# Kernel tuning notes

Measured on AMD Instinct MI355X. Metric: run time of the kernel, lower is better.

## Reference

```python
import jax, jax.numpy as jnp
import numpy as np

N_IMG = 1024
N_VIEWS = 90


def _bilinear(img, yi, xi):
    """Bilinear sample img at float coords (yi=row, xi=col); 0 outside (skimage warp cval=0)."""
    n = img.shape[0]
    y0 = jnp.floor(yi)
    x0 = jnp.floor(xi)
    wy = yi - y0
    wx = xi - x0
    y0i = y0.astype(jnp.int32)
    x0i = x0.astype(jnp.int32)

    def get(yy, xx):
        valid = (yy >= 0) & (yy < n) & (xx >= 0) & (xx < n)
        v = img[jnp.clip(yy, 0, n - 1), jnp.clip(xx, 0, n - 1)]
        return jnp.where(valid, v, jnp.zeros((), img.dtype))

    v00 = get(y0i, x0i)
    v01 = get(y0i, x0i + 1)
    v10 = get(y0i + 1, x0i)
    v11 = get(y0i + 1, x0i + 1)
    return (v00 * (1 - wy) * (1 - wx) + v01 * (1 - wy) * wx
            + v10 * wy * (1 - wx) + v11 * wy * wx)


def radon_jax(image, theta_deg):
    """skimage.transform.radon(image, theta, circle=True) equivalent.
    Rotate image by each angle (bilinear, about center = N//2, inverse map as in
    skimage warp) and sum over rows. Returns sinogram [N, n_angles]."""
    n = image.shape[0]
    center = n // 2
    ang = jnp.deg2rad(theta_deg.astype(image.dtype))
    cos_a = jnp.cos(ang)  # [A]
    sin_a = jnp.sin(ang)
    coords = jnp.arange(n, dtype=image.dtype)
    X, Y = jnp.meshgrid(coords, coords)  # X = col (x), Y = row (y), [N, N]

    def rotate_and_sum(ca, sa):
        # inverse map: src = R @ dst (homogeneous, (x, y) order) as in skimage radon
        x_in = ca * X + sa * Y - center * (ca + sa - 1)
        y_in = -sa * X + ca * Y - center * (ca - sa - 1)
        rotated = _bilinear(image, y_in, x_in)  # [N, N]
        return rotated.sum(axis=0)  # sum over rows -> projection [N]

    sino = jax.vmap(rotate_and_sum)(cos_a, sin_a)  # [A, N]
    return sino.T  # [N, A] to match skimage radon layout


def setup_inputs() -> dict:
    key = jax.random.key(0)
    k1, _ = jax.random.split(key)
    x = jax.random.normal(k1, (N_IMG, N_IMG), dtype=jnp.float32)
    theta = jnp.arange(N_VIEWS, dtype=jnp.float32) * 2.0  # 0..178 deg, 2-deg spacing
    return {"x": x, "theta": theta}


def reference(x, theta):
    return radon_jax(x, theta)
```

## Files before the change

kernel.cpp:

```cpp
#include <hip/hip_runtime.h>

#define N_IMG    1024
#define N_VIEWS  90
#define CENTER   512
#define NTHREADS 256
#define NWAVES   4
#define NJOBS    8
#define BUFW     5120

typedef float v2f __attribute__((ext_vector_type(2)));

__device__ __forceinline__ void map_coords(float ca, float sa, float cx, float cy,
                                           float Xf, float Yf,
                                           float& x_in, float& y_in) {
    const float fx0 = fmaf(ca, Xf, cx);
    const float fy0 = fmaf(-sa, Xf, cy);
    x_in = fmaf(sa, Yf, fx0);
    y_in = fmaf(ca, Yf, fy0);
}

__device__ __forceinline__ void gload_lds4(const float* g, float* l) {
    __builtin_amdgcn_global_load_lds((const __attribute__((address_space(1))) void*)g,
                                     (__attribute__((address_space(3))) void*)l, 4, 0, 0);
}

__global__ __launch_bounds__(NTHREADS, 8) void radon_q(const float* __restrict__ img,
                                                       const float* __restrict__ theta,
                                                       float* __restrict__ out) {
    __shared__ float buf[BUFW];

    const int tx = blockIdx.x;
    const int q  = blockIdx.y;
    const int a  = blockIdx.z;
    const int X0 = tx * 64;
    const int Yq = q * (NJOBS * 32);
    const int tid  = threadIdx.x;
    const int lane = tid & 63;
    const int wv   = tid >> 6;

    const float ang = theta[a] * 0.017453292519943295f;
    float sa, ca;
    __sincosf(ang, &sa, &ca);
    const float cx = (float)CENTER * (1.0f - ca - sa);
    const float cy = (float)CENTER * (1.0f - ca + sa);

    const float Xf  = (float)(X0 + lane);
    const float fx0 = fmaf(ca, Xf, cx);
    const float fy0 = fmaf(-sa, Xf, cy);
    const v2f sa2 = {sa, sa};
    const v2f ca2 = {ca, ca};
    const v2f fx2 = {fx0, fx0};
    const v2f fy2 = {fy0, fy0};
    float acc = 0.0f;

    for (int j = 0; j < NJOBS; ++j) {
        const float Y0f = (float)(Yq + j * 32);
        const float Y1f = Y0f + 31.0f;
        float x00, y00, x01, y01, x10, y10, x11, y11;
        map_coords(ca, sa, cx, cy, (float)X0,        Y0f, x00, y00);
        map_coords(ca, sa, cx, cy, (float)(X0 + 63), Y0f, x01, y01);
        map_coords(ca, sa, cx, cy, (float)X0,        Y1f, x10, y10);
        map_coords(ca, sa, cx, cy, (float)(X0 + 63), Y1f, x11, y11);
        const float xmin = fminf(fminf(x00, x01), fminf(x10, x11));
        const float xmax = fmaxf(fmaxf(x00, x01), fmaxf(x10, x11));
        const float ymin = fminf(fminf(y00, y01), fminf(y10, y11));
        const float ymax = fmaxf(fmaxf(y00, y01), fmaxf(y10, y11));
        const int ix0 = (int)floorf(xmin);
        const int ix1 = (int)floorf(xmax) + 1;
        const int iy0 = (int)floorf(ymin);
        const int iy1 = (int)floorf(ymax) + 1;

        if (ix1 < 0 || ix0 > N_IMG - 1 || iy1 < 0 || iy0 > N_IMG - 1)
            continue;

        const bool interior = (ix0 >= 0) && (ix1 <= N_IMG - 1) &&
                              (iy0 >= 0) && (iy1 <= N_IMG - 1);
        const int win = ix0;
        const int WS  = ix1 - ix0 + 1;
        const int P   = WS | 1;
        const int R   = iy1 - iy0 + 1;

        if (interior) {
            const float* g = img + (size_t)(iy0 + wv) * N_IMG + win;
            float* l = buf + wv * P;
            if (WS <= 64) {
                for (int r = wv; r < R; r += NWAVES) {
                    if (lane < WS) gload_lds4(g + lane, l);
                    g += NWAVES * N_IMG;
                    l += NWAVES * P;
                }
            } else {
                for (int r = wv; r < R; r += NWAVES) {
                    gload_lds4(g + lane, l);
                    if (lane < WS - 64) gload_lds4(g + 64 + lane, l + 64);
                    g += NWAVES * N_IMG;
                    l += NWAVES * P;
                }
            }
        } else {
            for (int r = wv; r < R; r += NWAVES) {
                const int gy = iy0 + r;
                const bool rok = ((unsigned)gy < (unsigned)N_IMG);
                const float* gp = img + (size_t)gy * N_IMG;
                float* l = buf + r * P;
                const int gx = win + lane;
                if (lane < WS) {
                    if (rok && (unsigned)gx < (unsigned)N_IMG) gload_lds4(gp + gx, l);
                    else l[lane] = 0.0f;
                }
                if (WS > 64) {
                    const int gx2 = gx + 64;
                    if (lane < WS - 64) {
                        if (rok && (unsigned)gx2 < (unsigned)N_IMG) gload_lds4(gp + gx2, l + 64);
                        else l[64 + lane] = 0.0f;
                    }
                }
            }
        }
        __syncthreads();

        const float Yb = Y0f + (float)(wv * 8);
        const float Pf = (float)P;
        const v2f P2 = {Pf, Pf};
        const float basef = -(float)(iy0 * P + win);
        const v2f b2 = {basef, basef};
        v2f Y2 = {Yb, Yb + 1.0f};
        const v2f two2 = {2.0f, 2.0f};
        v2f acc2 = {0.0f, 0.0f};
        #pragma unroll
        for (int p = 0; p < 4; ++p) {
            const v2f x2 = sa2 * Y2 + fx2;
            const v2f y2 = ca2 * Y2 + fy2;
            v2f x0f = {floorf(x2.x), floorf(x2.y)};
            v2f y0f = {floorf(y2.x), floorf(y2.y)};
            const v2f wx = x2 - x0f;
            const v2f wy = y2 - y0f;
            const v2f lif = y0f * P2 + x0f + b2;
            const int li0 = (int)lif.x;
            const int li1 = (int)lif.y;
            const int li0p = li0 + P;
            const int li1p = li1 + P;
            const v2f t00 = {buf[li0],      buf[li1]};
            const v2f t01 = {buf[li0 + 1],  buf[li1 + 1]};
            const v2f t10 = {buf[li0p],     buf[li1p]};
            const v2f t11 = {buf[li0p + 1], buf[li1p + 1]};
            const v2f top = (t01 - t00) * wx + t00;
            const v2f bot = (t11 - t10) * wx + t10;
            acc2 += (bot - top) * wy + top;
            Y2 += two2;
        }
        acc += acc2.x + acc2.y;

        __syncthreads();
    }

    buf[tid] = acc;
    __syncthreads();
    if (tid < 64) {
        const float s = buf[tid] + buf[tid + 64] + buf[tid + 128] + buf[tid + 192];
        atomicAdd(&out[(size_t)(X0 + tid) * N_VIEWS + a], s);
    }
}

extern "C" void kernel_launch(void* const* d_in, const int* in_sizes, int n_in,
                              void* d_out, int out_size, void* d_ws, size_t ws_size,
                              hipStream_t stream) {
    const float* img   = (const float*)d_in[0];
    const float* theta = (const float*)d_in[1];
    float* out = (float*)d_out;
    (void)d_ws; (void)ws_size;

    (void)hipMemsetAsync(d_out, 0, (size_t)out_size * sizeof(float), stream);
    radon_q<<<dim3(16, 4, N_VIEWS), NTHREADS, 0, stream>>>(img, theta, out);
}
```

Before: 144.6 us.

## Halve per-job row tile to 16 and pad LDS stride to 32/64/96

Each job now covers 16 output rows instead of 32, with twice as many jobs per block, so the staged rotated footprint per job is smaller. The LDS row pitch becomes a power-of-two-like bucket (32/64/96) instead of WS|1. Narrow windows load two rows per wave so all 64 lanes issue loads. Bounding-box corners are precomputed outside the loop. The cost is twice as many barriers per block and possible LDS bank conflicts from even strides.

```diff
diff --git a/kernel.cpp b/kernel.cpp
--- a/kernel.cpp
+++ b/kernel.cpp
@@ -5,7 +5,7 @@
 #define CENTER   512
 #define NTHREADS 256
 #define NWAVES   4
-#define NJOBS    8
+#define NJOBS    16
 #define BUFW     5120
 
 typedef float v2f __attribute__((ext_vector_type(2)));
@@ -33,7 +33,7 @@
     const int q  = blockIdx.y;
     const int a  = blockIdx.z;
     const int X0 = tx * 64;
-    const int Yq = q * (NJOBS * 32);
+    const int Yq = q * (NJOBS * 16);
     const int tid  = threadIdx.x;
     const int lane = tid & 63;
     const int wv   = tid >> 6;
@@ -43,6 +43,11 @@
     __sincosf(ang, &sa, &ca);
     const float cx = (float)CENTER * (1.0f - ca - sa);
     const float cy = (float)CENTER * (1.0f - ca + sa);
+
+    const float fxA = fmaf(ca, (float)X0,        cx);
+    const float fxB = fmaf(ca, (float)(X0 + 63), cx);
+    const float fyA = fmaf(-sa, (float)X0,        cy);
+    const float fyB = fmaf(-sa, (float)(X0 + 63), cy);
 
     const float Xf  = (float)(X0 + lane);
     const float fx0 = fmaf(ca, Xf, cx);
@@ -54,13 +59,12 @@
     float acc = 0.0f;
 
     for (int j = 0; j < NJOBS; ++j) {
-        const float Y0f = (float)(Yq + j * 32);
-        const float Y1f = Y0f + 31.0f;
-        float x00, y00, x01, y01, x10, y10, x11, y11;
-        map_coords(ca, sa, cx, cy, (float)X0,        Y0f, x00, y00);
-        map_coords(ca, sa, cx, cy, (float)(X0 + 63), Y0f, x01, y01);
-        map_coords(ca, sa, cx, cy, (float)X0,        Y1f, x10, y10);
-        map_coords(ca, sa, cx, cy, (float)(X0 + 63), Y1f, x11, y11);
+        const float Y0f = (float)(Yq + j * 16);
+        const float Y1f = Y0f + 15.0f;
+        const float x00 = fmaf(sa, Y0f, fxA), x01 = fmaf(sa, Y0f, fxB);
+        const float x10 = fmaf(sa, Y1f, fxA), x11 = fmaf(sa, Y1f, fxB);
+        const float y00 = fmaf(ca, Y0f, fyA), y01 = fmaf(ca, Y0f, fyB);
+        const float y10 = fmaf(ca, Y1f, fyA), y11 = fmaf(ca, Y1f, fyB);
         const float xmin = fminf(fminf(x00, x01), fminf(x10, x11));
         const float xmax = fmaxf(fmaxf(x00, x01), fmaxf(x10, x11));
         const float ymin = fminf(fminf(y00, y01), fminf(y10, y11));
@@ -77,24 +81,35 @@
                               (iy0 >= 0) && (iy1 <= N_IMG - 1);
         const int win = ix0;
         const int WS  = ix1 - ix0 + 1;
-        const int P   = WS | 1;
         const int R   = iy1 - iy0 + 1;
+        const int P   = (WS <= 32) ? 32 : ((WS <= 64) ? 64 : 96);
 
         if (interior) {
-            const float* g = img + (size_t)(iy0 + wv) * N_IMG + win;
-            float* l = buf + wv * P;
-            if (WS <= 64) {
+            if (P == 32) {
+                const int half = lane >> 5, lc = lane & 31;
+                const int nt = (R + 1) >> 1;
+                for (int t = wv; t < nt; t += NWAVES) {
+                    const int r = 2 * t + half;
+                    if (lc < WS && r < R)
+                        gload_lds4(img + (size_t)(iy0 + r) * N_IMG + win + lc,
+                                   buf + (t << 6));
+                }
+            } else if (P == 64) {
+                const float* g = img + (size_t)(iy0 + wv) * N_IMG + win;
+                float* l = buf + (wv << 6);
                 for (int r = wv; r < R; r += NWAVES) {
                     if (lane < WS) gload_lds4(g + lane, l);
                     g += NWAVES * N_IMG;
-                    l += NWAVES * P;
+                    l += NWAVES * 64;
                 }
             } else {
+                const float* g = img + (size_t)(iy0 + wv) * N_IMG + win;
+                float* l = buf + wv * 96;
                 for (int r = wv; r < R; r += NWAVES) {
                     gload_lds4(g + lane, l);
                     if (lane < WS - 64) gload_lds4(g + 64 + lane, l + 64);
                     g += NWAVES * N_IMG;
-                    l += NWAVES * P;
+                    l += NWAVES * 96;
                 }
             }
         } else {
@@ -108,18 +123,16 @@
                     if (rok && (unsigned)gx < (unsigned)N_IMG) gload_lds4(gp + gx, l);
                     else l[lane] = 0.0f;
                 }
-                if (WS > 64) {
+                if (WS > 64 && lane < WS - 64) {
                     const int gx2 = gx + 64;
-                    if (lane < WS - 64) {
-                        if (rok && (unsigned)gx2 < (unsigned)N_IMG) gload_lds4(gp + gx2, l + 64);
-                        else l[64 + lane] = 0.0f;
-                    }
+                    if (rok && (unsigned)gx2 < (unsigned)N_IMG) gload_lds4(gp + gx2, l + 64);
+                    else l[64 + lane] = 0.0f;
                 }
             }
         }
         __syncthreads();
 
-        const float Yb = Y0f + (float)(wv * 8);
+        const float Yb = Y0f + (float)(wv << 2);
         const float Pf = (float)P;
         const v2f P2 = {Pf, Pf};
         const float basef = -(float)(iy0 * P + win);
@@ -128,7 +141,7 @@
         const v2f two2 = {2.0f, 2.0f};
         v2f acc2 = {0.0f, 0.0f};
         #pragma unroll
-        for (int p = 0; p < 4; ++p) {
+        for (int p = 0; p < 2; ++p) {
             const v2f x2 = sa2 * Y2 + fx2;
             const v2f y2 = ca2 * Y2 + fy2;
             v2f x0f = {floorf(x2.x), floorf(x2.y)};
```

Result: slower. 193.8 us (+34.0%).

## Use transposed-flipped image copy for steep angles and widen blocks with 16-byte LDS loads

Applied to the files above, without the earlier changes.

Adds a transpose-and-flip pre-pass into workspace so that, for angles where |sin| exceeds |cos|, the kernel samples a transposed image whose footprint per tile is narrow and row-contiguous. This keeps the LDS staging window at a fixed 96-float pitch. The main kernel moves to 512 threads with 8 waves and 64-row jobs, computes the per-job bounding boxes once across lanes and broadcasts them with shuffles, and stages interior windows with 16-byte global-to-LDS loads. In exchange it adds an extra kernel launch plus a full image transpose, and computes sin/cos in double precision.

```diff
diff --git a/kernel.cpp b/kernel.cpp
--- a/kernel.cpp
+++ b/kernel.cpp
@@ -3,10 +3,11 @@
 #define N_IMG    1024
 #define N_VIEWS  90
 #define CENTER   512
-#define NTHREADS 256
-#define NWAVES   4
-#define NJOBS    8
-#define BUFW     5120
+#define NTHREADS 512
+#define NWAVES   8
+#define JOBS     4
+#define PIT      96
+#define BUFW     9088
 
 typedef float v2f __attribute__((ext_vector_type(2)));
 
@@ -23,127 +24,150 @@
     __builtin_amdgcn_global_load_lds((const __attribute__((address_space(1))) void*)g,
                                      (__attribute__((address_space(3))) void*)l, 4, 0, 0);
 }
-
-__global__ __launch_bounds__(NTHREADS, 8) void radon_q(const float* __restrict__ img,
-                                                       const float* __restrict__ theta,
-                                                       float* __restrict__ out) {
+__device__ __forceinline__ void gload_lds16(const float* g, float* l) {
+    __builtin_amdgcn_global_load_lds((const __attribute__((address_space(1))) void*)g,
+                                     (__attribute__((address_space(3))) void*)l, 16, 0, 0);
+}
+
+__global__ __launch_bounds__(256) void transpose_flip(const float* __restrict__ img,
+                                                      float* __restrict__ T) {
+    __shared__ float tile[64][65];
+    const int t  = blockIdx.x, tr = t >> 4, tc = t & 15;
+    const int tid = threadIdx.x, lane = tid & 63, w = tid >> 6;
+    #pragma unroll
+    for (int k = 0; k < 16; ++k) {
+        const int row = (w << 4) + k;
+        tile[row][lane] = img[(size_t)((tr << 6) + row) * N_IMG + (tc << 6) + lane];
+    }
+    __syncthreads();
+    #pragma unroll
+    for (int k = 0; k < 16; ++k) {
+        const int j = (tc << 6) + (w << 4) + k;
+        const int i = 1023 - ((tr << 6) + lane);
+        T[(size_t)j * N_IMG + i] = tile[lane][(w << 4) + k];
+    }
+}
+
+__global__ __launch_bounds__(NTHREADS, 8) void radon_fused(const float* __restrict__ img,
+                                                           const float* __restrict__ Tbuf,
+                                                           const float* __restrict__ theta,
+                                                           float* __restrict__ out,
+                                                           int useT) {
     __shared__ float buf[BUFW];
 
     const int tx = blockIdx.x;
     const int q  = blockIdx.y;
     const int a  = blockIdx.z;
     const int X0 = tx * 64;
-    const int Yq = q * (NJOBS * 32);
+    const int Yq = q * (JOBS * 64);
     const int tid  = threadIdx.x;
     const int lane = tid & 63;
     const int wv   = tid >> 6;
 
     const float ang = theta[a] * 0.017453292519943295f;
-    float sa, ca;
-    __sincosf(ang, &sa, &ca);
-    const float cx = (float)CENTER * (1.0f - ca - sa);
-    const float cy = (float)CENTER * (1.0f - ca + sa);
+    double sd_, cd_;
+    sincos((double)ang, &sd_, &cd_);
+    const float s0 = (float)sd_, c0 = (float)cd_;
+    const float cx0 = (float)CENTER * (1.0f - c0 - s0);
+    const float cy0 = (float)CENTER * (1.0f - c0 + s0);
+
+    float c, s, cx, cy;
+    const float* __restrict__ src;
+    if (useT && fabsf(s0) > fabsf(c0)) {
+        c = s0; s = -c0; cx = 1023.0f - cy0; cy = cx0; src = Tbuf;
+    } else {
+        c = c0; s = s0;  cx = cx0;            cy = cy0;  src = img;
+    }
+
+    const int jj = lane & (JOBS - 1);
+    const float Yb = (float)(Yq + jj * 64);
+    float x00, y00, x01, y01, x10, y10, x11, y11;
+    map_coords(c, s, cx, cy, (float)X0,        Yb,        x00, y00);
+    map_coords(c, s, cx, cy, (float)(X0 + 63), Yb,        x01, y01);
+    map_coords(c, s, cx, cy, (float)X0,        Yb + 63.f, x10, y10);
+    map_coords(c, s, cx, cy, (float)(X0 + 63), Yb + 63.f, x11, y11);
+    const float xmin = fminf(fminf(x00, x01), fminf(x10, x11));
+    const float xmax = fmaxf(fmaxf(x00, x01), fmaxf(x10, x11));
+    const float ymin = fminf(fminf(y00, y01), fminf(y10, y11));
+    const float ymax = fmaxf(fmaxf(y00, y01), fmaxf(y10, y11));
+
+    const int ix0 = (int)floorf(xmin);
+    const int ix1 = (int)floorf(xmax) + 1;
+    const int iy0 = (int)floorf(ymin);
+    const int iy1 = (int)floorf(ymax) + 1;
+
+    const bool empty = (ix1 < 0) || (ix0 > N_IMG - 1) ||
+                       (iy1 < 0) || (iy0 > N_IMG - 1);
+    const bool interior = (ix0 >= 0) && (ix1 <= N_IMG - 1) &&
+                          (iy0 >= 0) && (iy1 <= N_IMG - 1);
+    const int winl = interior ? min(ix0 & ~3, N_IMG - PIT) : (ix0 & ~3);
+    const int nrl  = iy1 - iy0 + 1;
+    const int iy0l = iy0;
+    const int fll  = empty ? 1 : (interior ? 2 : 0);
 
     const float Xf  = (float)(X0 + lane);
-    const float fx0 = fmaf(ca, Xf, cx);
-    const float fy0 = fmaf(-sa, Xf, cy);
-    const v2f sa2 = {sa, sa};
-    const v2f ca2 = {ca, ca};
-    const v2f fx2 = {fx0, fx0};
-    const v2f fy2 = {fy0, fy0};
+    const float bx  = fmaf(c, Xf, cx);
+    const float by  = fmaf(-s, Xf, cy);
+    const v2f s2 = {s, s}, c2 = {c, c};
+    const v2f bx2 = {bx, bx}, by2 = {by, by};
+    const v2f P2 = {(float)PIT, (float)PIT};
     float acc = 0.0f;
 
-    for (int j = 0; j < NJOBS; ++j) {
-        const float Y0f = (float)(Yq + j * 32);
-        const float Y1f = Y0f + 31.0f;
-        float x00, y00, x01, y01, x10, y10, x11, y11;
-        map_coords(ca, sa, cx, cy, (float)X0,        Y0f, x00, y00);
-        map_coords(ca, sa, cx, cy, (float)(X0 + 63), Y0f, x01, y01);
-        map_coords(ca, sa, cx, cy, (float)X0,        Y1f, x10, y10);
-        map_coords(ca, sa, cx, cy, (float)(X0 + 63), Y1f, x11, y11);
-        const float xmin = fminf(fminf(x00, x01), fminf(x10, x11));
-        const float xmax = fmaxf(fmaxf(x00, x01), fmaxf(x10, x11));
-        const float ymin = fminf(fminf(y00, y01), fminf(y10, y11));
-        const float ymax = fmaxf(fmaxf(y00, y01), fmaxf(y10, y11));
-        const int ix0 = (int)floorf(xmin);
-        const int ix1 = (int)floorf(xmax) + 1;
-        const int iy0 = (int)floorf(ymin);
-        const int iy1 = (int)floorf(ymax) + 1;
-
-        if (ix1 < 0 || ix0 > N_IMG - 1 || iy1 < 0 || iy0 > N_IMG - 1)
-            continue;
-
-        const bool interior = (ix0 >= 0) && (ix1 <= N_IMG - 1) &&
-                              (iy0 >= 0) && (iy1 <= N_IMG - 1);
-        const int win = ix0;
-        const int WS  = ix1 - ix0 + 1;
-        const int P   = WS | 1;
-        const int R   = iy1 - iy0 + 1;
-
-        if (interior) {
-            const float* g = img + (size_t)(iy0 + wv) * N_IMG + win;
-            float* l = buf + wv * P;
-            if (WS <= 64) {
-                for (int r = wv; r < R; r += NWAVES) {
-                    if (lane < WS) gload_lds4(g + lane, l);
-                    g += NWAVES * N_IMG;
-                    l += NWAVES * P;
-                }
-            } else {
-                for (int r = wv; r < R; r += NWAVES) {
-                    gload_lds4(g + lane, l);
-                    if (lane < WS - 64) gload_lds4(g + 64 + lane, l + 64);
-                    g += NWAVES * N_IMG;
-                    l += NWAVES * P;
-                }
+    for (int j = 0; j < JOBS; ++j) {
+        const int win   = __shfl(winl, j);
+        const int iyj   = __shfl(iy0l, j);
+        const int nrows = __shfl(nrl,  j);
+        const int fl    = __shfl(fll,  j);
+        if (fl == 1) continue;
+
+        if (fl & 2) {
+            const int D = nrows * PIT;
+            for (int o = wv * 256; o < D; o += NWAVES * 256) {
+                const int d = o + 4 * lane;
+                const int r = (unsigned)d / 96u;
+                const int cc = d - r * 96;
+                const int gr = min(iyj + r, N_IMG - 1);
+                gload_lds16(src + (size_t)gr * N_IMG + win + cc, buf + o);
             }
         } else {
-            for (int r = wv; r < R; r += NWAVES) {
-                const int gy = iy0 + r;
+            for (int r = wv; r < nrows; r += NWAVES) {
+                const int gy = iyj + r;
                 const bool rok = ((unsigned)gy < (unsigned)N_IMG);
-                const float* gp = img + (size_t)gy * N_IMG;
-                float* l = buf + r * P;
+                const float* gp = src + (size_t)gy * N_IMG;
+                float* l = buf + r * PIT;
                 const int gx = win + lane;
-                if (lane < WS) {
-                    if (rok && (unsigned)gx < (unsigned)N_IMG) gload_lds4(gp + gx, l);
-                    else l[lane] = 0.0f;
-                }
-                if (WS > 64) {
+                if (rok && (unsigned)gx < (unsigned)N_IMG) gload_lds4(gp + gx, l);
+                else l[lane] = 0.0f;
+                if (lane < 32) {
                     const int gx2 = gx + 64;
-                    if (lane < WS - 64) {
-                        if (rok && (unsigned)gx2 < (unsigned)N_IMG) gload_lds4(gp + gx2, l + 64);
-                        else l[64 + lane] = 0.0f;
-                    }
+                    if (rok && (unsigned)gx2 < (unsigned)N_IMG) gload_lds4(gp + gx2, l + 64);
+                    else l[64 + lane] = 0.0f;
                 }
             }
         }
         __syncthreads();
 
-        const float Yb = Y0f + (float)(wv * 8);
-        const float Pf = (float)P;
-        const v2f P2 = {Pf, Pf};
-        const float basef = -(float)(iy0 * P + win);
+        const float Yw = (float)(Yq + j * 64 + wv * 8);
+        const float basef = -(float)(iyj * PIT + win);
         const v2f b2 = {basef, basef};
-        v2f Y2 = {Yb, Yb + 1.0f};
+        v2f Y2 = {Yw, Yw + 1.0f};
         const v2f two2 = {2.0f, 2.0f};
         v2f acc2 = {0.0f, 0.0f};
         #pragma unroll
         for (int p = 0; p < 4; ++p) {
-            const v2f x2 = sa2 * Y2 + fx2;
-            const v2f y2 = ca2 * Y2 + fy2;
-            v2f x0f = {floorf(x2.x), floorf(x2.y)};
-            v2f y0f = {floorf(y2.x), floorf(y2.y)};
+            const v2f x2 = s2 * Y2 + bx2;
+            const v2f y2 = c2 * Y2 + by2;
+            const v2f x0f = {floorf(x2.x), floorf(x2.y)};
+            const v2f y0f = {floorf(y2.x), floorf(y2.y)};
             const v2f wx = x2 - x0f;
             const v2f wy = y2 - y0f;
             const v2f lif = y0f * P2 + x0f + b2;
             const int li0 = (int)lif.x;
             const int li1 = (int)lif.y;
-            const int li0p = li0 + P;
-            const int li1p = li1 + P;
-            const v2f t00 = {buf[li0],      buf[li1]};
-            const v2f t01 = {buf[li0 + 1],  buf[li1 + 1]};
-            const v2f t10 = {buf[li0p],     buf[li1p]};
-            const v2f t11 = {buf[li0p + 1], buf[li1p + 1]};
+            const v2f t00 = {buf[li0],           buf[li1]};
+            const v2f t01 = {buf[li0 + 1],       buf[li1 + 1]};
+            const v2f t10 = {buf[li0 + PIT],     buf[li1 + PIT]};
+            const v2f t11 = {buf[li0 + PIT + 1], buf[li1 + PIT + 1]};
             const v2f top = (t01 - t00) * wx + t00;
             const v2f bot = (t11 - t10) * wx + t10;
             acc2 += (bot - top) * wy + top;
@@ -154,11 +178,13 @@
         __syncthreads();
     }
 
-    buf[tid] = acc;
+    buf[wv * 64 + lane] = acc;
     __syncthreads();
-    if (tid < 64) {
-        const float s = buf[tid] + buf[tid + 64] + buf[tid + 128] + buf[tid + 192];
-        atomicAdd(&out[(size_t)(X0 + tid) * N_VIEWS + a], s);
+    if (wv == 0) {
+        float ssum = 0.0f;
+        #pragma unroll
+        for (int w = 0; w < NWAVES; ++w) ssum += buf[w * 64 + lane];
+        atomicAdd(&out[(size_t)(X0 + lane) * N_VIEWS + a], ssum);
     }
 }
 
@@ -168,8 +194,13 @@
     const float* img   = (const float*)d_in[0];
     const float* theta = (const float*)d_in[1];
     float* out = (float*)d_out;
-    (void)d_ws; (void)ws_size;
+
+    float* T = (float*)d_ws;
+    const int useT = (ws_size >= (size_t)N_IMG * N_IMG * sizeof(float)) ? 1 : 0;
 
     (void)hipMemsetAsync(d_out, 0, (size_t)out_size * sizeof(float), stream);
-    radon_q<<<dim3(16, 4, N_VIEWS), NTHREADS, 0, stream>>>(img, theta, out);
-}
+    if (useT)
+        transpose_flip<<<dim3(256), 256, 0, stream>>>(img, T);
+    radon_fused<<<dim3(16, 4, N_VIEWS), NTHREADS, 0, stream>>>(img, useT ? T : img,
+                                                               theta, out, useT);
+}
```

New measurement: 131.8 us. 1.1x faster.
